# Optimization experiments

Measured on AMD Instinct MI355X. Metric: run time of the kernel, lower is better.

Reference implementation:

```python
import jax, jax.numpy as jnp
import numpy as np

N_NODE = 10000
E = 320000
E_LINK = 1280000
D = 128            # emb_input_dim = n_factors*delta_d = hid_dim
EDGE_FEAT = 24     # 2 + ceil(64/3)
SEQ = 64
K = 3


def _propagate(x, src, dst, w, n_seg):
    # out[d] = sum_{e: dst[e]=d} w[e] * x[src[e]]  (sparse matvec via gather-scatter)
    return jax.ops.segment_sum(w[:, None] * x[src], dst, num_segments=n_seg)


def setup_inputs() -> dict:
    key = jax.random.key(0)
    ks = jax.random.split(key, 16)
    inp = {
        "h_entity": jax.random.normal(ks[0], (SEQ, N_NODE, D), dtype=jnp.float32),
        "x_link": jax.random.normal(ks[1], (E, EDGE_FEAT), dtype=jnp.float32),
        "edge_weight_link": jax.random.uniform(ks[2], (E_LINK,), dtype=jnp.float32),
        "edge_index_link": jax.random.randint(ks[3], (2, E_LINK), 0, E, dtype=jnp.int32),
        "edge_index": jax.random.randint(ks[4], (2, E), 0, N_NODE, dtype=jnp.int32),
    }
    s = 0.05
    inp.update({
        "W_start": jax.random.normal(ks[5], (EDGE_FEAT, D), dtype=jnp.float32) * s,
        "b_start": jnp.zeros((D,), jnp.float32),
        "W_hl": jax.random.normal(ks[6], (K, D, D), dtype=jnp.float32) * s,
        "b_hl": jnp.zeros((D,), jnp.float32),
        "W_ec": jax.random.normal(ks[7], (D, K * 2), dtype=jnp.float32) * s,
        "b_ec": jnp.zeros((K * 2,), jnp.float32),
        "W_t": jax.random.normal(ks[8], (SEQ, 1), dtype=jnp.float32) * s,
        "b_t": jnp.zeros((1,), jnp.float32),
        "W_gcn": jax.random.normal(ks[9], (K, D, D), dtype=jnp.float32) * s,
        "b_gcn": jnp.zeros((D,), jnp.float32),
    })
    return inp


def reference(h_entity, x_link, edge_weight_link, W_start, b_start, W_hl, b_hl,
              W_ec, b_ec, W_t, b_t, W_gcn, b_gcn, edge_index_link, edge_index):
    src_l, dst_l = edge_index_link[0], edge_index_link[1]
    src_n, dst_n = edge_index[0], edge_index[1]

    # start_mlp_edge
    h_link = x_link @ W_start + b_start                      # [E, D]

    # HodgeLaguerreConv, K=3: Laguerre polynomial recurrence on edge Laplacian L
    # Tx0 = x; Tx1 = (1 - L)x; Tx_{k+1} = ((2k+1-L)Tx_k - k Tx_{k-1})/(k+1)
    Tx0 = h_link
    out_e = Tx0 @ W_hl[0]
    Tx1 = Tx0 - _propagate(Tx0, src_l, dst_l, edge_weight_link, E)
    out_e = out_e + Tx1 @ W_hl[1]
    Tx2 = (3.0 * Tx1 - _propagate(Tx1, src_l, dst_l, edge_weight_link, E) - Tx0) * 0.5
    out_e = out_e + Tx2 @ W_hl[2] + b_hl                     # [E, D]

    # per-edge causal scores, K*2 columns
    score = out_e @ W_ec + b_ec                              # [E, 2K]

    # temporal projection: [T,N,D] -> permute -> [N,D,T] @ [T,1] -> [N,D]
    h_ent = jnp.einsum('tnd,t->nd', h_entity, W_t[:, 0]) + b_t[0]

    # K-hop GCN: hop-k edge weight = softmax over the (causal, non-causal) pair k
    w_k = jax.nn.softmax(score.reshape(E, K, 2), axis=-1)[..., 0]  # [E, K]
    h = h_ent
    out_n = jnp.zeros((N_NODE, D), dtype=h_ent.dtype)
    for k in range(K):
        h = _propagate(h, src_n, dst_n, w_k[:, k], N_NODE)
        out_n = out_n + h @ W_gcn[k]
    out_n = out_n + b_gcn
    return out_n
```

## Files before the change

### kernel.cpp

```cpp
#include <hip/hip_runtime.h>

#define N_NODE   10000
#define E_EDGE   320000
#define E_LINKN  1280000
#define DIM      128
#define EFEAT    24
#define SEQLEN   64

#define SCAN_CHUNK 4096

static const size_t OFF_DEGN  = 0;
static const size_t OFF_CURN  = OFF_DEGN  + 10240*4;
static const size_t OFF_DEGL  = OFF_CURN  + 10240*4;
static const size_t OFF_CURL  = OFF_DEGL  + (size_t)E_EDGE*4;
static const size_t ZERO_BYTES= OFF_CURL  + (size_t)E_EDGE*4;
static const size_t OFF_CONST = ZERO_BYTES;
static const size_t OFF_V0    = OFF_CONST + 512*4;
static const size_t OFF_V12   = OFF_V0    + (size_t)E_EDGE*6*4;
static const size_t OFF_PW    = OFF_V12   + (size_t)E_EDGE*12*4;
static const size_t OFF_WSUM  = OFF_PW    + (size_t)E_EDGE*12*4;
static const size_t OFF_STARTN= OFF_WSUM  + (size_t)E_EDGE*4;
static const size_t OFF_SRCSN = OFF_STARTN+ 10304*4;
static const size_t OFF_POSN  = OFF_SRCSN + (size_t)E_EDGE*4;
static const size_t OFF_WKS   = OFF_POSN  + (size_t)E_EDGE*4;
static const size_t OFF_STARTL= OFF_WKS   + (size_t)E_EDGE*3*4;
static const size_t OFF_SRCSL = OFF_STARTL+ ((size_t)E_EDGE+64)*4;
static const size_t OFF_WL    = OFF_SRCSL + (size_t)E_LINKN*4;
static const size_t OFF_HENT  = OFF_WL    + (size_t)E_LINKN*4;
static const size_t OFF_HA    = OFF_HENT  + (size_t)N_NODE*DIM*4;
static const size_t OFF_HB    = OFF_HA    + (size_t)N_NODE*DIM*4;
static const size_t OFF_PARTN = OFF_HB    + (size_t)N_NODE*DIM*4;
static const size_t OFF_PARTL = OFF_PARTN + 512*4;

__global__ void consts_kernel(const float* __restrict__ Wstart, const float* __restrict__ bstart,
                              const float* __restrict__ Whl,    const float* __restrict__ bhl,
                              const float* __restrict__ Wec,    const float* __restrict__ bec,
                              float* __restrict__ Ball, float* __restrict__ cvec) {
    __shared__ float M[128*129];
    __shared__ float sWec[768];
    __shared__ float A[768];
    int k = blockIdx.x;
    int t = threadIdx.x;

    for (int i = t; i < 768; i += 256) sWec[i] = Wec[i];

    const float* w0 = Whl;
    const float* w1 = Whl + 16384;
    const float* w2 = Whl + 32768;
    for (int idx = t; idx < 16384; idx += 256) {
        int r = idx >> 7, d = idx & 127;
        float m;
        if (k == 0)      m = w0[idx] + w1[idx] + w2[idx];
        else if (k == 1) m = -(w1[idx] + 2.f*w2[idx]);
        else             m = 0.5f * w2[idx];
        M[r*129 + d] = m;
    }
    __syncthreads();

    for (int idx = t; idx < 768; idx += 256) {
        int r = idx / 6, j = idx % 6;
        float s = 0.f;
        for (int d = 0; d < 128; d++) s += M[r*129 + d] * sWec[d*6 + j];
        A[idx] = s;
    }
    __syncthreads();

    if (t < 144) {
        int i = t / 6, j = t % 6;
        float s = 0.f;
        for (int r = 0; r < 128; r++) s += Wstart[i*128 + r] * A[r*6 + j];
        Ball[i*18 + k*6 + j] = s;
    } else if (t < 150) {
        int j = t - 144;
        float s = 0.f;
        for (int r = 0; r < 128; r++) s += bstart[r] * A[r*6 + j];
        cvec[k*6 + j] = s;
    } else if (k == 0 && t >= 160 && t < 166) {
        int j = t - 160;
        float s = bec[j];
        for (int d = 0; d < 128; d++) s += bhl[d] * sWec[d*6 + j];
        cvec[18 + j] = s;
    }
}

__global__ void v_kernel(const float* __restrict__ x, const float* __restrict__ Ball,
                         float* __restrict__ V0, float* __restrict__ V12) {
    __shared__ float sB[432];
    for (int i = threadIdx.x; i < 432; i += blockDim.x) sB[i] = Ball[i];
    __syncthreads();
    int e = blockIdx.x * blockDim.x + threadIdx.x;
    if (e >= E_EDGE) return;
    float xr[24];
    const float4* xp = (const float4*)(x + (size_t)e*24);
#pragma unroll
    for (int q = 0; q < 6; q++) {
        float4 v = xp[q];
        xr[4*q+0] = v.x; xr[4*q+1] = v.y; xr[4*q+2] = v.z; xr[4*q+3] = v.w;
    }
    float o[18];
#pragma unroll
    for (int j = 0; j < 18; j++) o[j] = 0.f;
#pragma unroll
    for (int i = 0; i < 24; i++) {
        float xv = xr[i];
#pragma unroll
        for (int j = 0; j < 18; j++) o[j] += xv * sB[i*18 + j];
    }
#pragma unroll
    for (int j = 0; j < 6; j++)  V0[(size_t)e*6 + j]  = o[j];
#pragma unroll
    for (int j = 0; j < 12; j++) V12[(size_t)e*12 + j] = o[6 + j];
}

__global__ void hist_kernel(const int* __restrict__ dst, int* __restrict__ deg, int n) {
    int e = blockIdx.x * blockDim.x + threadIdx.x;
    if (e < n) atomicAdd(deg + dst[e], 1);
}

__global__ void partial_kernel(const int* __restrict__ deg, int* __restrict__ partials, int n) {
    __shared__ int red[256];
    int b = blockIdx.x, t = threadIdx.x;
    int base = b * SCAN_CHUNK;
    int s = 0;
    for (int i = t; i < SCAN_CHUNK; i += 256) {
        int idx = base + i;
        if (idx < n) s += deg[idx];
    }
    red[t] = s;
    __syncthreads();
    for (int off = 128; off > 0; off >>= 1) {
        if (t < off) red[t] += red[t + off];
        __syncthreads();
    }
    if (t == 0) partials[b] = red[0];
}

__global__ void scan_partials_kernel(const int* __restrict__ partials, int* __restrict__ offs,
                                     int* __restrict__ start, int nb, int n) {
    __shared__ int a[256];
    int t = threadIdx.x;
    a[t] = (t < nb) ? partials[t] : 0;
    __syncthreads();
    for (int off = 1; off < 256; off <<= 1) {
        int v = (t >= off) ? a[t - off] : 0;
        __syncthreads();
        a[t] += v;
        __syncthreads();
    }
    offs[t] = (t == 0) ? 0 : a[t - 1];
    if (t == 255) start[n] = a[nb - 1];
}

__global__ void scan_block_kernel(const int* __restrict__ deg, const int* __restrict__ offs,
                                  int* __restrict__ start, int n) {
    __shared__ int s[SCAN_CHUNK];
    __shared__ int tsum[256];
    int b = blockIdx.x, t = threadIdx.x;
    int base = b * SCAN_CHUNK;
    for (int i = t; i < SCAN_CHUNK; i += 256) {
        int idx = base + i;
        s[i] = (idx < n) ? deg[idx] : 0;
    }
    __syncthreads();
    int lo = t * 16;
    int mysum = 0;
#pragma unroll
    for (int j = 0; j < 16; j++) mysum += s[lo + j];
    tsum[t] = mysum;
    __syncthreads();
    for (int off = 1; off < 256; off <<= 1) {
        int v = (t >= off) ? tsum[t - off] : 0;
        __syncthreads();
        tsum[t] += v;
        __syncthreads();
    }
    int run = offs[b] + ((t == 0) ? 0 : tsum[t - 1]);
#pragma unroll
    for (int j = 0; j < 16; j++) {
        int v = s[lo + j];
        s[lo + j] = run;
        run += v;
    }
    __syncthreads();
    for (int i = t; i < SCAN_CHUNK; i += 256) {
        int idx = base + i;
        if (idx < n) start[idx] = s[i];
    }
}

__global__ void fill_n_kernel(const int* __restrict__ srcn, const int* __restrict__ dstn,
                              const int* __restrict__ start, int* __restrict__ cursor,
                              int* __restrict__ srcs_srt, int* __restrict__ pos) {
    int e = blockIdx.x * blockDim.x + threadIdx.x;
    if (e >= E_EDGE) return;
    int d = dstn[e];
    int p = start[d] + atomicAdd(cursor + d, 1);
    srcs_srt[p] = srcn[e];
    pos[e] = p;
}

__global__ void fill_l_kernel(const int* __restrict__ srcl, const int* __restrict__ dstl,
                              const float* __restrict__ ew,
                              const int* __restrict__ start, int* __restrict__ cursor,
                              int* __restrict__ srcs_srt, float* __restrict__ w_srt) {
    int e = blockIdx.x * blockDim.x + threadIdx.x;
    if (e >= E_LINKN) return;
    int d = dstl[e];
    int p = start[d] + atomicAdd(cursor + d, 1);
    srcs_srt[p] = srcl[e];
    w_srt[p] = ew[e];
}

__global__ void prop1_gather(const float* __restrict__ V12, const int* __restrict__ startl,
                             const int* __restrict__ srcsl, const float* __restrict__ wl,
                             float* __restrict__ PW, float* __restrict__ wsum) {
    int e = blockIdx.x * blockDim.x + threadIdx.x;
    if (e >= E_EDGE) return;
    int s0 = startl[e], s1 = startl[e + 1];
    float acc[12];
#pragma unroll
    for (int j = 0; j < 12; j++) acc[j] = 0.f;
    float ws = 0.f;
    for (int j = s0; j < s1; j++) {
        int s = srcsl[j];
        float w = wl[j];
        const float4* vp = (const float4*)(V12 + (size_t)s*12);
#pragma unroll
        for (int q = 0; q < 3; q++) {
            float4 v = vp[q];
            acc[4*q+0] += w*v.x; acc[4*q+1] += w*v.y;
            acc[4*q+2] += w*v.z; acc[4*q+3] += w*v.w;
        }
        ws += w;
    }
    float4* pw = (float4*)(PW + (size_t)e*12);
#pragma unroll
    for (int q = 0; q < 3; q++)
        pw[q] = make_float4(acc[4*q+0], acc[4*q+1], acc[4*q+2], acc[4*q+3]);
    wsum[e] = ws;
}

__global__ void prop2score_kernel(const float* __restrict__ PW, const float* __restrict__ wsum,
                                  const int* __restrict__ startl, const int* __restrict__ srcsl,
                                  const float* __restrict__ wl, const float* __restrict__ V0,
                                  const float* __restrict__ cvec, const int* __restrict__ posn,
                                  float* __restrict__ wks) {
    __shared__ float sc[24];
    if (threadIdx.x < 24) sc[threadIdx.x] = cvec[threadIdx.x];
    __syncthreads();
    int e = blockIdx.x * blockDim.x + threadIdx.x;
    if (e >= E_EDGE) return;
    int s0 = startl[e], s1 = startl[e + 1];
    float p2[6];
#pragma unroll
    for (int j = 0; j < 6; j++) p2[j] = 0.f;
    float ws2 = 0.f;
    for (int j = s0; j < s1; j++) {
        int s = srcsl[j];
        float w = wl[j];
        const float2* pv = (const float2*)(PW + (size_t)s*12 + 6);
#pragma unroll
        for (int q = 0; q < 3; q++) {
            float2 v = pv[q];
            p2[2*q+0] += w*v.x; p2[2*q+1] += w*v.y;
        }
        ws2 += w * wsum[s];
    }
    float ws1 = wsum[e];
    float S[6];
#pragma unroll
    for (int j = 0; j < 6; j++)
        S[j] = V0[(size_t)e*6 + j] + PW[(size_t)e*12 + j] + p2[j]
             + ws1*sc[6 + j] + ws2*sc[12 + j] + sc[j] + sc[18 + j];
    int p = posn[e];
#pragma unroll
    for (int k = 0; k < 3; k++)
        wks[(size_t)p*3 + k] = 1.f / (1.f + __expf(S[2*k+1] - S[2*k]));
}

__global__ void temporal_kernel(const float4* __restrict__ h_entity, const float* __restrict__ Wt,
                                const float* __restrict__ bt, float4* __restrict__ h_ent) {
    __shared__ float sw[SEQLEN];
    if (threadIdx.x < SEQLEN) sw[threadIdx.x] = Wt[threadIdx.x];
    __syncthreads();
    int i = blockIdx.x * blockDim.x + threadIdx.x;
    if (i >= N_NODE*DIM/4) return;
    float b = bt[0];
    float4 acc = make_float4(b, b, b, b);
#pragma unroll 8
    for (int t = 0; t < SEQLEN; t++) {
        float4 v = h_entity[(size_t)t * (N_NODE*DIM/4) + i];
        float w = sw[t];
        acc.x += w*v.x; acc.y += w*v.y; acc.z += w*v.z; acc.w += w*v.w;
    }
    h_ent[i] = acc;
}

__global__ void hop_kernel(const float* __restrict__ h_cur, float* __restrict__ h_next,
                           float* __restrict__ out,
                           const int* __restrict__ startn, const int* __restrict__ srcs_srt,
                           const float* __restrict__ wks, int k,
                           const float* __restrict__ G, const float* __restrict__ bgcn, int first) {
    int node = blockIdx.x;
    int tid  = threadIdx.x;
    int s0 = startn[node], s1 = startn[node + 1];
    float acc = 0.f;
    for (int j = s0; j < s1; j++) {
        float w = wks[(size_t)j*3 + k];
        int sn = srcs_srt[j];
        acc += w * h_cur[(size_t)sn*DIM + tid];
    }
    h_next[(size_t)node*DIM + tid] = acc;
    __shared__ float hrow[DIM];
    hrow[tid] = acc;
    __syncthreads();
    float o = first ? bgcn[tid] : out[(size_t)node*DIM + tid];
#pragma unroll 8
    for (int d = 0; d < DIM; d++) o += hrow[d] * G[d*DIM + tid];
    out[(size_t)node*DIM + tid] = o;
}

extern "C" void kernel_launch(void* const* d_in, const int* in_sizes, int n_in,
                              void* d_out, int out_size, void* d_ws, size_t ws_size,
                              hipStream_t stream) {
    const float* h_entity = (const float*)d_in[0];
    const float* x_link   = (const float*)d_in[1];
    const float* ewl      = (const float*)d_in[2];
    const int*   eil      = (const int*)d_in[3];
    const int*   ein      = (const int*)d_in[4];
    const float* Wstart   = (const float*)d_in[5];
    const float* bstart   = (const float*)d_in[6];
    const float* Whl      = (const float*)d_in[7];
    const float* bhl      = (const float*)d_in[8];
    const float* Wec      = (const float*)d_in[9];
    const float* bec      = (const float*)d_in[10];
    const float* Wt       = (const float*)d_in[11];
    const float* bt       = (const float*)d_in[12];
    const float* Wgcn     = (const float*)d_in[13];
    const float* bgcn     = (const float*)d_in[14];
    float* out = (float*)d_out;
    char*  ws  = (char*)d_ws;

    const int* srcl = eil;
    const int* dstl = eil + E_LINKN;
    const int* srcn = ein;
    const int* dstn = ein + E_EDGE;

    int*   degn  = (int*)  (ws + OFF_DEGN);
    int*   curn  = (int*)  (ws + OFF_CURN);
    int*   degl  = (int*)  (ws + OFF_DEGL);
    int*   curl  = (int*)  (ws + OFF_CURL);
    float* Ball  = (float*)(ws + OFF_CONST);
    float* cvec  = Ball + 432;
    float* V0    = (float*)(ws + OFF_V0);
    float* V12   = (float*)(ws + OFF_V12);
    float* PW    = (float*)(ws + OFF_PW);
    float* wsum  = (float*)(ws + OFF_WSUM);
    int*   startn= (int*)  (ws + OFF_STARTN);
    int*   srcsn = (int*)  (ws + OFF_SRCSN);
    int*   posn  = (int*)  (ws + OFF_POSN);
    float* wks   = (float*)(ws + OFF_WKS);
    int*   startl= (int*)  (ws + OFF_STARTL);
    int*   srcsl = (int*)  (ws + OFF_SRCSL);
    float* wl    = (float*)(ws + OFF_WL);
    float* h_ent = (float*)(ws + OFF_HENT);
    float* h_a   = (float*)(ws + OFF_HA);
    float* h_b   = (float*)(ws + OFF_HB);
    int*   partn = (int*)  (ws + OFF_PARTN);
    int*   partl = (int*)  (ws + OFF_PARTL);

    const int nbN = (N_NODE + SCAN_CHUNK - 1) / SCAN_CHUNK;
    const int nbL = (E_EDGE + SCAN_CHUNK - 1) / SCAN_CHUNK;

    hipMemsetAsync(ws, 0, ZERO_BYTES, stream);

    consts_kernel<<<3, 256, 0, stream>>>(Wstart, bstart, Whl, bhl, Wec, bec, Ball, cvec);
    v_kernel<<<(E_EDGE + 255)/256, 256, 0, stream>>>(x_link, Ball, V0, V12);

    hist_kernel<<<(E_EDGE + 255)/256, 256, 0, stream>>>(dstn, degn, E_EDGE);
    hist_kernel<<<(E_LINKN + 255)/256, 256, 0, stream>>>(dstl, degl, E_LINKN);

    partial_kernel<<<nbN, 256, 0, stream>>>(degn, partn, N_NODE);
    scan_partials_kernel<<<1, 256, 0, stream>>>(partn, partn + 256, startn, nbN, N_NODE);
    scan_block_kernel<<<nbN, 256, 0, stream>>>(degn, partn + 256, startn, N_NODE);

    partial_kernel<<<nbL, 256, 0, stream>>>(degl, partl, E_EDGE);
    scan_partials_kernel<<<1, 256, 0, stream>>>(partl, partl + 256, startl, nbL, E_EDGE);
    scan_block_kernel<<<nbL, 256, 0, stream>>>(degl, partl + 256, startl, E_EDGE);

    fill_n_kernel<<<(E_EDGE + 255)/256, 256, 0, stream>>>(srcn, dstn, startn, curn, srcsn, posn);
    fill_l_kernel<<<(E_LINKN + 255)/256, 256, 0, stream>>>(srcl, dstl, ewl, startl, curl, srcsl, wl);

    prop1_gather<<<(E_EDGE + 255)/256, 256, 0, stream>>>(V12, startl, srcsl, wl, PW, wsum);
    prop2score_kernel<<<(E_EDGE + 255)/256, 256, 0, stream>>>(PW, wsum, startl, srcsl, wl,
                                                             V0, cvec, posn, wks);

    temporal_kernel<<<(N_NODE*DIM/4 + 255)/256, 256, 0, stream>>>(
        (const float4*)h_entity, Wt, bt, (float4*)h_ent);

    hop_kernel<<<N_NODE, DIM, 0, stream>>>(h_ent, h_a, out, startn, srcsn, wks, 0,
                                           Wgcn + 0*16384, bgcn, 1);
    hop_kernel<<<N_NODE, DIM, 0, stream>>>(h_a, h_b, out, startn, srcsn, wks, 1,
                                           Wgcn + 1*16384, bgcn, 0);
    hop_kernel<<<N_NODE, DIM, 0, stream>>>(h_b, h_ent, out, startn, srcsn, wks, 2,
                                           Wgcn + 2*16384, bgcn, 0);
}
```

Measured before the change: 967.5 us.

## Pad edge feature rows, pack link src/weight, split hop GEMM into tiled kernel

Pads V12 and PW rows to 16 floats so gathers use aligned float4 loads, and folds the weight-sum into the padded PW row. Packs the sorted link source index and weight into one int2 array and prefetches the next entry in the gather loops. Stores the three hop weights as one float4 per edge. Moves the per-node 128x128 GEMV out of the hop kernels into a single shared-memory tiled GEMM over all three hops. The per-node GEMV reloaded the weight matrix from global memory for every node. The cost is extra workspace and memory traffic from the padding, plus one more N×D buffer.

```diff
diff --git a/kernel.cpp b/kernel.cpp
--- a/kernel.cpp
+++ b/kernel.cpp
@@ -17,19 +17,18 @@
 static const size_t OFF_CONST = ZERO_BYTES;
 static const size_t OFF_V0    = OFF_CONST + 512*4;
 static const size_t OFF_V12   = OFF_V0    + (size_t)E_EDGE*6*4;
-static const size_t OFF_PW    = OFF_V12   + (size_t)E_EDGE*12*4;
-static const size_t OFF_WSUM  = OFF_PW    + (size_t)E_EDGE*12*4;
-static const size_t OFF_STARTN= OFF_WSUM  + (size_t)E_EDGE*4;
+static const size_t OFF_PW    = OFF_V12   + (size_t)E_EDGE*16*4;
+static const size_t OFF_STARTN= OFF_PW    + (size_t)E_EDGE*16*4;
 static const size_t OFF_SRCSN = OFF_STARTN+ 10304*4;
 static const size_t OFF_POSN  = OFF_SRCSN + (size_t)E_EDGE*4;
-static const size_t OFF_WKS   = OFF_POSN  + (size_t)E_EDGE*4;
-static const size_t OFF_STARTL= OFF_WKS   + (size_t)E_EDGE*3*4;
-static const size_t OFF_SRCSL = OFF_STARTL+ ((size_t)E_EDGE+64)*4;
-static const size_t OFF_WL    = OFF_SRCSL + (size_t)E_LINKN*4;
-static const size_t OFF_HENT  = OFF_WL    + (size_t)E_LINKN*4;
+static const size_t OFF_WKS4  = OFF_POSN  + (size_t)E_EDGE*4;
+static const size_t OFF_STARTL= OFF_WKS4  + (size_t)E_EDGE*16;
+static const size_t OFF_LSW   = OFF_STARTL+ ((size_t)E_EDGE+64)*4;
+static const size_t OFF_HENT  = OFF_LSW   + (size_t)E_LINKN*8;
 static const size_t OFF_HA    = OFF_HENT  + (size_t)N_NODE*DIM*4;
 static const size_t OFF_HB    = OFF_HA    + (size_t)N_NODE*DIM*4;
-static const size_t OFF_PARTN = OFF_HB    + (size_t)N_NODE*DIM*4;
+static const size_t OFF_HC    = OFF_HB    + (size_t)N_NODE*DIM*4;
+static const size_t OFF_PARTN = OFF_HC    + (size_t)N_NODE*DIM*4;
 static const size_t OFF_PARTL = OFF_PARTN + 512*4;
 
 __global__ void consts_kernel(const float* __restrict__ Wstart, const float* __restrict__ bstart,
@@ -106,10 +105,14 @@
 #pragma unroll
         for (int j = 0; j < 18; j++) o[j] += xv * sB[i*18 + j];
     }
-#pragma unroll
-    for (int j = 0; j < 6; j++)  V0[(size_t)e*6 + j]  = o[j];
-#pragma unroll
-    for (int j = 0; j < 12; j++) V12[(size_t)e*12 + j] = o[6 + j];
+    float2* v0p = (float2*)(V0 + (size_t)e*6);
+    v0p[0] = make_float2(o[0], o[1]);
+    v0p[1] = make_float2(o[2], o[3]);
+    v0p[2] = make_float2(o[4], o[5]);
+    float4* v12p = (float4*)(V12 + (size_t)e*16);
+    v12p[0] = make_float4(o[6],  o[7],  o[8],  o[9]);
+    v12p[1] = make_float4(o[10], o[11], o[12], o[13]);
+    v12p[2] = make_float4(o[14], o[15], o[16], o[17]);
 }
 
 __global__ void hist_kernel(const int* __restrict__ dst, int* __restrict__ deg, int n) {
@@ -202,18 +205,16 @@
 __global__ void fill_l_kernel(const int* __restrict__ srcl, const int* __restrict__ dstl,
                               const float* __restrict__ ew,
                               const int* __restrict__ start, int* __restrict__ cursor,
-                              int* __restrict__ srcs_srt, float* __restrict__ w_srt) {
+                              int2* __restrict__ lsw) {
     int e = blockIdx.x * blockDim.x + threadIdx.x;
     if (e >= E_LINKN) return;
     int d = dstl[e];
     int p = start[d] + atomicAdd(cursor + d, 1);
-    srcs_srt[p] = srcl[e];
-    w_srt[p] = ew[e];
+    lsw[p] = make_int2(srcl[e], __float_as_int(ew[e]));
 }
 
 __global__ void prop1_gather(const float* __restrict__ V12, const int* __restrict__ startl,
-                             const int* __restrict__ srcsl, const float* __restrict__ wl,
-                             float* __restrict__ PW, float* __restrict__ wsum) {
+                             const int2* __restrict__ lsw, float* __restrict__ PW) {
     int e = blockIdx.x * blockDim.x + threadIdx.x;
     if (e >= E_EDGE) return;
     int s0 = startl[e], s1 = startl[e + 1];
@@ -221,10 +222,12 @@
 #pragma unroll
     for (int j = 0; j < 12; j++) acc[j] = 0.f;
     float ws = 0.f;
+    int2 cur = make_int2(0, 0);
+    if (s0 < s1) cur = lsw[s0];
     for (int j = s0; j < s1; j++) {
-        int s = srcsl[j];
-        float w = wl[j];
-        const float4* vp = (const float4*)(V12 + (size_t)s*12);
+        int2 nxt = (j + 1 < s1) ? lsw[j + 1] : cur;
+        float w = __int_as_float(cur.y);
+        const float4* vp = (const float4*)(V12 + (size_t)cur.x*16);
 #pragma unroll
         for (int q = 0; q < 3; q++) {
             float4 v = vp[q];
@@ -232,19 +235,20 @@
             acc[4*q+2] += w*v.z; acc[4*q+3] += w*v.w;
         }
         ws += w;
-    }
-    float4* pw = (float4*)(PW + (size_t)e*12);
-#pragma unroll
-    for (int q = 0; q < 3; q++)
-        pw[q] = make_float4(acc[4*q+0], acc[4*q+1], acc[4*q+2], acc[4*q+3]);
-    wsum[e] = ws;
-}
-
-__global__ void prop2score_kernel(const float* __restrict__ PW, const float* __restrict__ wsum,
-                                  const int* __restrict__ startl, const int* __restrict__ srcsl,
-                                  const float* __restrict__ wl, const float* __restrict__ V0,
+        cur = nxt;
+    }
+    float4* pw = (float4*)(PW + (size_t)e*16);
+    pw[0] = make_float4(acc[0], acc[1], acc[2],  acc[3]);
+    pw[1] = make_float4(acc[4], acc[5], acc[6],  acc[7]);
+    pw[2] = make_float4(acc[8], acc[9], acc[10], acc[11]);
+    pw[3] = make_float4(ws, 0.f, 0.f, 0.f);
+}
+
+__global__ void prop2score_kernel(const float* __restrict__ PW,
+                                  const int* __restrict__ startl, const int2* __restrict__ lsw,
+                                  const float* __restrict__ V0,
                                   const float* __restrict__ cvec, const int* __restrict__ posn,
-                                  float* __restrict__ wks) {
+                                  float4* __restrict__ wks4) {
     __shared__ float sc[24];
     if (threadIdx.x < 24) sc[threadIdx.x] = cvec[threadIdx.x];
     __syncthreads();
@@ -255,27 +259,38 @@
 #pragma unroll
     for (int j = 0; j < 6; j++) p2[j] = 0.f;
     float ws2 = 0.f;
+    int2 cur = make_int2(0, 0);
+    if (s0 < s1) cur = lsw[s0];
     for (int j = s0; j < s1; j++) {
-        int s = srcsl[j];
-        float w = wl[j];
-        const float2* pv = (const float2*)(PW + (size_t)s*12 + 6);
-#pragma unroll
-        for (int q = 0; q < 3; q++) {
-            float2 v = pv[q];
-            p2[2*q+0] += w*v.x; p2[2*q+1] += w*v.y;
-        }
-        ws2 += w * wsum[s];
-    }
-    float ws1 = wsum[e];
+        int2 nxt = (j + 1 < s1) ? lsw[j + 1] : cur;
+        float w = __int_as_float(cur.y);
+        const float4* pv = (const float4*)(PW + (size_t)cur.x*16);
+        float4 a = pv[1];
+        float4 b = pv[2];
+        float4 c = pv[3];
+        p2[0] += w*a.z; p2[1] += w*a.w;
+        p2[2] += w*b.x; p2[3] += w*b.y; p2[4] += w*b.z; p2[5] += w*b.w;
+        ws2 += w * c.x;
+        cur = nxt;
+    }
+    const float4* pe = (const float4*)(PW + (size_t)e*16);
+    float4 q0 = pe[0];
+    float4 q1 = pe[1];
+    float  ws1 = pe[3].x;
+    float pw6[6] = {q0.x, q0.y, q0.z, q0.w, q1.x, q1.y};
+    const float2* v0p = (const float2*)(V0 + (size_t)e*6);
+    float2 f0 = v0p[0], f1 = v0p[1], f2 = v0p[2];
+    float v0r[6] = {f0.x, f0.y, f1.x, f1.y, f2.x, f2.y};
     float S[6];
 #pragma unroll
     for (int j = 0; j < 6; j++)
-        S[j] = V0[(size_t)e*6 + j] + PW[(size_t)e*12 + j] + p2[j]
+        S[j] = v0r[j] + pw6[j] + p2[j]
              + ws1*sc[6 + j] + ws2*sc[12 + j] + sc[j] + sc[18 + j];
     int p = posn[e];
-#pragma unroll
-    for (int k = 0; k < 3; k++)
-        wks[(size_t)p*3 + k] = 1.f / (1.f + __expf(S[2*k+1] - S[2*k]));
+    float w0 = 1.f / (1.f + __expf(S[1] - S[0]));
+    float w1 = 1.f / (1.f + __expf(S[3] - S[2]));
+    float w2 = 1.f / (1.f + __expf(S[5] - S[4]));
+    wks4[p] = make_float4(w0, w1, w2, 0.f);
 }
 
 __global__ void temporal_kernel(const float4* __restrict__ h_entity, const float* __restrict__ Wt,
@@ -296,28 +311,74 @@
     h_ent[i] = acc;
 }
 
-__global__ void hop_kernel(const float* __restrict__ h_cur, float* __restrict__ h_next,
-                           float* __restrict__ out,
-                           const int* __restrict__ startn, const int* __restrict__ srcs_srt,
-                           const float* __restrict__ wks, int k,
-                           const float* __restrict__ G, const float* __restrict__ bgcn, int first) {
+__global__ void prop_hop(const float* __restrict__ h_cur, float* __restrict__ h_next,
+                         const int* __restrict__ startn, const int* __restrict__ srcs_srt,
+                         const float4* __restrict__ wks4, int k) {
     int node = blockIdx.x;
     int tid  = threadIdx.x;
     int s0 = startn[node], s1 = startn[node + 1];
     float acc = 0.f;
     for (int j = s0; j < s1; j++) {
-        float w = wks[(size_t)j*3 + k];
+        float4 wv = wks4[j];
+        float w = (k == 0) ? wv.x : (k == 1) ? wv.y : wv.z;
         int sn = srcs_srt[j];
         acc += w * h_cur[(size_t)sn*DIM + tid];
     }
     h_next[(size_t)node*DIM + tid] = acc;
-    __shared__ float hrow[DIM];
-    hrow[tid] = acc;
-    __syncthreads();
-    float o = first ? bgcn[tid] : out[(size_t)node*DIM + tid];
-#pragma unroll 8
-    for (int d = 0; d < DIM; d++) o += hrow[d] * G[d*DIM + tid];
-    out[(size_t)node*DIM + tid] = o;
+}
+
+__global__ void __launch_bounds__(256)
+gemm_final(const float* __restrict__ h1, const float* __restrict__ h2,
+           const float* __restrict__ h3, const float* __restrict__ Wgcn,
+           const float* __restrict__ bgcn, float* __restrict__ out) {
+    __shared__ float sG[128*128];
+    __shared__ float sh[32*128];
+    int t = threadIdx.x;
+    int cg = t & 31, rg = t >> 5;
+    int c0 = cg * 4, r0 = rg * 4;
+    int rbase = blockIdx.x * 32;
+    int nrows = N_NODE - rbase; if (nrows > 32) nrows = 32;
+
+    float4 bb = *(const float4*)(bgcn + c0);
+    float acc[4][4];
+#pragma unroll
+    for (int r = 0; r < 4; r++) {
+        acc[r][0] = bb.x; acc[r][1] = bb.y; acc[r][2] = bb.z; acc[r][3] = bb.w;
+    }
+
+    const float* hs0[3] = {h1, h2, h3};
+    for (int k = 0; k < 3; k++) {
+        __syncthreads();
+        const float4* gk = (const float4*)(Wgcn + (size_t)k*16384);
+        float4* sg4 = (float4*)sG;
+        for (int i = t; i < 4096; i += 256) sg4[i] = gk[i];
+        const float4* hg = (const float4*)(hs0[k] + (size_t)rbase*128);
+        float4* sh4 = (float4*)sh;
+        for (int i = t; i < 1024; i += 256)
+            sh4[i] = ((i >> 5) < nrows) ? hg[i] : make_float4(0.f, 0.f, 0.f, 0.f);
+        __syncthreads();
+#pragma unroll 2
+        for (int d4 = 0; d4 < 32; d4++) {
+            float4 g0 = *(const float4*)(sG + (d4*4 + 0)*128 + c0);
+            float4 g1 = *(const float4*)(sG + (d4*4 + 1)*128 + c0);
+            float4 g2 = *(const float4*)(sG + (d4*4 + 2)*128 + c0);
+            float4 g3 = *(const float4*)(sG + (d4*4 + 3)*128 + c0);
+#pragma unroll
+            for (int r = 0; r < 4; r++) {
+                float4 hv = *(const float4*)(sh + (r0 + r)*128 + d4*4);
+                acc[r][0] += hv.x*g0.x; acc[r][1] += hv.x*g0.y; acc[r][2] += hv.x*g0.z; acc[r][3] += hv.x*g0.w;
+                acc[r][0] += hv.y*g1.x; acc[r][1] += hv.y*g1.y; acc[r][2] += hv.y*g1.z; acc[r][3] += hv.y*g1.w;
+                acc[r][0] += hv.z*g2.x; acc[r][1] += hv.z*g2.y; acc[r][2] += hv.z*g2.z; acc[r][3] += hv.z*g2.w;
+                acc[r][0] += hv.w*g3.x; acc[r][1] += hv.w*g3.y; acc[r][2] += hv.w*g3.z; acc[r][3] += hv.w*g3.w;
+            }
+        }
+    }
+#pragma unroll
+    for (int r = 0; r < 4; r++) {
+        if (r0 + r < nrows)
+            *(float4*)(out + (size_t)(rbase + r0 + r)*128 + c0) =
+                make_float4(acc[r][0], acc[r][1], acc[r][2], acc[r][3]);
+    }
 }
 
 extern "C" void kernel_launch(void* const* d_in, const int* in_sizes, int n_in,
@@ -346,28 +407,27 @@
     const int* srcn = ein;
     const int* dstn = ein + E_EDGE;
 
-    int*   degn  = (int*)  (ws + OFF_DEGN);
-    int*   curn  = (int*)  (ws + OFF_CURN);
-    int*   degl  = (int*)  (ws + OFF_DEGL);
-    int*   curl  = (int*)  (ws + OFF_CURL);
-    float* Ball  = (float*)(ws + OFF_CONST);
-    float* cvec  = Ball + 432;
-    float* V0    = (float*)(ws + OFF_V0);
-    float* V12   = (float*)(ws + OFF_V12);
-    float* PW    = (float*)(ws + OFF_PW);
-    float* wsum  = (float*)(ws + OFF_WSUM);
-    int*   startn= (int*)  (ws + OFF_STARTN);
-    int*   srcsn = (int*)  (ws + OFF_SRCSN);
-    int*   posn  = (int*)  (ws + OFF_POSN);
-    float* wks   = (float*)(ws + OFF_WKS);
-    int*   startl= (int*)  (ws + OFF_STARTL);
-    int*   srcsl = (int*)  (ws + OFF_SRCSL);
-    float* wl    = (float*)(ws + OFF_WL);
-    float* h_ent = (float*)(ws + OFF_HENT);
-    float* h_a   = (float*)(ws + OFF_HA);
-    float* h_b   = (float*)(ws + OFF_HB);
-    int*   partn = (int*)  (ws + OFF_PARTN);
-    int*   partl = (int*)  (ws + OFF_PARTL);
+    int*    degn  = (int*)   (ws + OFF_DEGN);
+    int*    curn  = (int*)   (ws + OFF_CURN);
+    int*    degl  = (int*)   (ws + OFF_DEGL);
+    int*    curl  = (int*)   (ws + OFF_CURL);
+    float*  Ball  = (float*) (ws + OFF_CONST);
+    float*  cvec  = Ball + 432;
+    float*  V0    = (float*) (ws + OFF_V0);
+    float*  V12   = (float*) (ws + OFF_V12);
+    float*  PW    = (float*) (ws + OFF_PW);
+    int*    startn= (int*)   (ws + OFF_STARTN);
+    int*    srcsn = (int*)   (ws + OFF_SRCSN);
+    int*    posn  = (int*)   (ws + OFF_POSN);
+    float4* wks4  = (float4*)(ws + OFF_WKS4);
+    int*    startl= (int*)   (ws + OFF_STARTL);
+    int2*   lsw   = (int2*)  (ws + OFF_LSW);
+    float*  h_ent = (float*) (ws + OFF_HENT);
+    float*  h_a   = (float*) (ws + OFF_HA);
+    float*  h_b   = (float*) (ws + OFF_HB);
+    float*  h_c   = (float*) (ws + OFF_HC);
+    int*    partn = (int*)   (ws + OFF_PARTN);
+    int*    partl = (int*)   (ws + OFF_PARTL);
 
     const int nbN = (N_NODE + SCAN_CHUNK - 1) / SCAN_CHUNK;
     const int nbL = (E_EDGE + SCAN_CHUNK - 1) / SCAN_CHUNK;
@@ -389,19 +449,18 @@
     scan_block_kernel<<<nbL, 256, 0, stream>>>(degl, partl + 256, startl, E_EDGE);
 
     fill_n_kernel<<<(E_EDGE + 255)/256, 256, 0, stream>>>(srcn, dstn, startn, curn, srcsn, posn);
-    fill_l_kernel<<<(E_LINKN + 255)/256, 256, 0, stream>>>(srcl, dstl, ewl, startl, curl, srcsl, wl);
-
-    prop1_gather<<<(E_EDGE + 255)/256, 256, 0, stream>>>(V12, startl, srcsl, wl, PW, wsum);
-    prop2score_kernel<<<(E_EDGE + 255)/256, 256, 0, stream>>>(PW, wsum, startl, srcsl, wl,
-                                                             V0, cvec, posn, wks);
+    fill_l_kernel<<<(E_LINKN + 255)/256, 256, 0, stream>>>(srcl, dstl, ewl, startl, curl, lsw);
+
+    prop1_gather<<<(E_EDGE + 255)/256, 256, 0, stream>>>(V12, startl, lsw, PW);
+    prop2score_kernel<<<(E_EDGE + 255)/256, 256, 0, stream>>>(PW, startl, lsw, V0, cvec,
+                                                              posn, wks4);
 
     temporal_kernel<<<(N_NODE*DIM/4 + 255)/256, 256, 0, stream>>>(
         (const float4*)h_entity, Wt, bt, (float4*)h_ent);
 
-    hop_kernel<<<N_NODE, DIM, 0, stream>>>(h_ent, h_a, out, startn, srcsn, wks, 0,
-                                           Wgcn + 0*16384, bgcn, 1);
-    hop_kernel<<<N_NODE, DIM, 0, stream>>>(h_a, h_b, out, startn, srcsn, wks, 1,
-                                           Wgcn + 1*16384, bgcn, 0);
-    hop_kernel<<<N_NODE, DIM, 0, stream>>>(h_b, h_ent, out, startn, srcsn, wks, 2,
-                                           Wgcn + 2*16384, bgcn, 0);
-}
+    prop_hop<<<N_NODE, DIM, 0, stream>>>(h_ent, h_a, startn, srcsn, wks4, 0);
+    prop_hop<<<N_NODE, DIM, 0, stream>>>(h_a,   h_b, startn, srcsn, wks4, 1);
+    prop_hop<<<N_NODE, DIM, 0, stream>>>(h_b,   h_c, startn, srcsn, wks4, 2);
+
+    gemm_final<<<(N_NODE + 31)/32, 256, 0, stream>>>(h_a, h_b, h_c, Wgcn, bgcn, out);
+}
```

New measurement: 953.7 us. No clear change (-1.4%).
